# Optimization experiments

Hardware: AMD Instinct MI355X
Metric: run time of the kernel (lower is better)

Reference implementation:

```python
import jax, jax.numpy as jnp
from jax import lax
import numpy as np

B, C, O, K, H, W = 32, 64, 64, 3, 128, 128
COND = 16
DN = ('NCHW', 'OIHW', 'NCHW')


def setup_inputs() -> dict:
    key = jax.random.key(0)
    ks = jax.random.split(key, 12)
    def rn(k, shape, fan_in):
        return jax.random.normal(k, shape, dtype=jnp.float32) / np.sqrt(fan_in)
    return {
        "x": jax.random.normal(ks[0], (B, C, H, W), dtype=jnp.float32),
        # condition_generator: Conv2d(C,16,3,stride=2) -> pool -> relu -> Conv2d(16,16,1) -> relu
        "cg_w1": rn(ks[1], (COND, C, 3, 3), C * 9),
        "cg_b1": jnp.zeros((COND,), jnp.float32),
        "cg_w2": rn(ks[2], (COND, COND), COND),
        "cg_b2": jnp.zeros((COND,), jnp.float32),
        # weight_generator: Conv2d(16, C*K*K, 1) + ReLU
        "wg_w": rn(ks[3], (C * K * K, COND), COND),
        "wg_b": 0.1 * jax.random.normal(ks[4], (C * K * K,), dtype=jnp.float32),
        # pointwise_generator: Conv2d(16, C*O, 1) + ReLU  (channels viewed as [O, C])
        "pg_w": rn(ks[5], (C * O, COND), COND),
        "pg_b": 0.1 * jax.random.normal(ks[6], (C * O,), dtype=jnp.float32),
        # bias_generator: Conv2d(16, O, 1)
        "bg_w": rn(ks[7], (O, COND), COND),
        "bg_b": jnp.zeros((O,), jnp.float32),
        # BatchNorm2d(O) affine params (training-mode batch stats)
        "bn_gamma": jnp.ones((O,), jnp.float32),
        "bn_beta": jnp.zeros((O,), jnp.float32),
    }


def reference(x, cg_w1, cg_b1, cg_w2, cg_b2, wg_w, wg_b, pg_w, pg_b,
              bg_w, bg_b, bn_gamma, bn_beta):
    b, c, h, w = x.shape
    # ---- condition generator: conv3x3 s2 (VALID) -> global avgpool -> relu -> 1x1 -> relu
    cond = lax.conv_general_dilated(x, cg_w1, (2, 2), 'VALID', dimension_numbers=DN)
    cond = cond + cg_b1[None, :, None, None]
    cond = cond.mean(axis=(2, 3))                      # [B,16] (AdaptiveAvgPool2d(1))
    cond = jax.nn.relu(cond)
    cond = jax.nn.relu(cond @ cg_w2.T + cg_b2)         # [B,16]
    # ---- per-sample dynamic weights
    dw = jax.nn.relu(cond @ wg_w.T + wg_b).reshape(b, c, 1, K, K)   # depthwise [B,C,1,K,K]
    pw = jax.nn.relu(cond @ pg_w.T + pg_b).reshape(b, O, c)         # pointwise [B,O,C]
    dbias = cond @ bg_w.T + bg_b                                    # [B,O]
    # ---- per-sample depthwise conv (stride=1, padding=1), vmapped over batch
    def dwconv(xi, ki):  # xi [C,H,W], ki [C,1,K,K]
        return lax.conv_general_dilated(xi[None], ki, (1, 1), [(1, 1), (1, 1)],
                                        feature_group_count=c,
                                        dimension_numbers=DN)[0]
    y = jax.vmap(dwconv)(x, dw)                        # [B,C,H,W]
    # ---- per-sample pointwise 1x1 conv + dynamic bias
    out = jnp.einsum('bchw,boc->bohw', y, pw) + dbias[:, :, None, None]
    # ---- BatchNorm2d (training mode: batch statistics over N,H,W)
    mean = out.mean(axis=(0, 2, 3))
    var = out.var(axis=(0, 2, 3))
    out = (out - mean[None, :, None, None]) * lax.rsqrt(var[None, :, None, None] + 1e-5)
    out = out * bn_gamma[None, :, None, None] + bn_beta[None, :, None, None]
    return out
```

## Files before the change

### kernel.cpp

```cpp
#include <hip/hip_runtime.h>

#define B_ 32
#define C_ 64
#define O_ 64
#define H_ 128
#define W_ 128

typedef __attribute__((ext_vector_type(8))) short short8;
typedef __attribute__((ext_vector_type(4))) float f32x4;

static __device__ __forceinline__ unsigned short f2bf(float f) {
    unsigned u = __builtin_bit_cast(unsigned, f);
    unsigned r = (u + 0x7FFFu + ((u >> 16) & 1u)) >> 16;
    return (unsigned short)r;
}

#define WS_S      0
#define WS_COND2  18432
#define WS_DW     18944
#define WS_DBIAS  37376
#define WS_PWBF   39424
#define WS_PSUM   104960
#define WS_PSQ    236032
#define WS_SCALE  367104
#define WS_SHIFT  367168

__global__ void __launch_bounds__(256) k_strided_sums(const float* __restrict__ x,
                                                      float* __restrict__ Sout) {
    int t = threadIdx.x;
    int bc = blockIdx.x;
    const float4* xp = (const float4*)(x + (size_t)bc * (H_ * W_));
    float a[9];
#pragma unroll
    for (int k = 0; k < 9; k++) a[k] = 0.f;
#pragma unroll
    for (int k = 0; k < 16; k++) {
        int i4 = t + k * 256;
        int h = i4 >> 5;
        int w0 = (i4 & 31) << 2;
        float4 v = xp[i4];
        float mA = (w0 == 124) ? 0.f : 1.f;
        float mB = (w0 == 0) ? 0.f : 1.f;
        float rs0 = v.x + mA * v.z;
        float rs1 = v.y + mA * v.w;
        float rs2 = mB * v.x + v.z;
        float e  = (h & 1) ? 0.f : 1.f;
        float od = 1.f - e;
        float hm0 = (h == 126) ? 0.f : e;
        float hm2 = (h == 0)   ? 0.f : e;
        float hm1 = (h == 127) ? 0.f : od;
        a[0] = fmaf(hm0, rs0, a[0]); a[1] = fmaf(hm0, rs1, a[1]); a[2] = fmaf(hm0, rs2, a[2]);
        a[3] = fmaf(hm1, rs0, a[3]); a[4] = fmaf(hm1, rs1, a[4]); a[5] = fmaf(hm1, rs2, a[5]);
        a[6] = fmaf(hm2, rs0, a[6]); a[7] = fmaf(hm2, rs1, a[7]); a[8] = fmaf(hm2, rs2, a[8]);
    }
    __shared__ float red[4][9];
    int lane = t & 63, wv = t >> 6;
#pragma unroll
    for (int k = 0; k < 9; k++) {
        float v = a[k];
        for (int off = 32; off > 0; off >>= 1) v += __shfl_down(v, off);
        if (lane == 0) red[wv][k] = v;
    }
    __syncthreads();
    if (t < 9) Sout[(size_t)bc * 9 + t] = red[0][t] + red[1][t] + red[2][t] + red[3][t];
}

__global__ void __launch_bounds__(256) k_cond(const float* __restrict__ S,
                       const float* __restrict__ w1, const float* __restrict__ b1,
                       const float* __restrict__ w2, const float* __restrict__ b2,
                       float* __restrict__ cond2) {
    int b = blockIdx.x;
    int t = threadIdx.x;
    int j = t >> 4, seg = t & 15;
    const float* Sb = S + b * 576;
    const float* w1j = w1 + j * 576;
    int i0 = seg * 36;
    float s = 0.f;
#pragma unroll 4
    for (int i = 0; i < 36; i++) s = fmaf(Sb[i0 + i], w1j[i0 + i], s);
    __shared__ float red[16][16];
    __shared__ float condv[16];
    red[j][seg] = s;
    __syncthreads();
    if (t < 16) {
        float acc = 0.f;
#pragma unroll
        for (int k = 0; k < 16; k++) acc += red[t][k];
        acc = acc * (1.f / 3969.f) + b1[t];
        condv[t] = fmaxf(acc, 0.f);
    }
    __syncthreads();
    if (t < 16) {
        float s2 = b2[t];
#pragma unroll
        for (int k = 0; k < 16; k++) s2 = fmaf(condv[k], w2[t * 16 + k], s2);
        cond2[b * 16 + t] = fmaxf(s2, 0.f);
    }
}

__global__ void k_dyn(const float* __restrict__ cond2,
                      const float* __restrict__ wg_w, const float* __restrict__ wg_b,
                      const float* __restrict__ pg_w, const float* __restrict__ pg_b,
                      const float* __restrict__ bg_w, const float* __restrict__ bg_b,
                      float* __restrict__ dw, unsigned short* __restrict__ pwbf,
                      float* __restrict__ dbias) {
    int idx = blockIdx.x * 256 + threadIdx.x;
    if (idx < 18432) {
        int b = idx / 576, r = idx - b * 576;
        const float* cd = cond2 + b * 16;
        float s = wg_b[r];
#pragma unroll
        for (int j = 0; j < 16; j++) s += cd[j] * wg_w[r * 16 + j];
        dw[idx] = fmaxf(s, 0.f);
    } else if (idx < 18432 + 131072) {
        int k = idx - 18432;
        int b = k >> 12, r = k & 4095;
        const float* cd = cond2 + b * 16;
        float s = pg_b[r];
#pragma unroll
        for (int j = 0; j < 16; j++) s += cd[j] * pg_w[r * 16 + j];
        pwbf[k] = f2bf(fmaxf(s, 0.f));
    } else if (idx < 151552) {
        int k = idx - 149504;
        int b = k >> 6, r = k & 63;
        const float* cd = cond2 + b * 16;
        float s = bg_b[r];
#pragma unroll
        for (int j = 0; j < 16; j++) s += cd[j] * bg_w[r * 16 + j];
        dbias[k] = s;
    }
}

struct SM4 {
    union {
        unsigned short y[256 * 72];
        float epi[32 * 260];
    };
    float xr[4 * 4 * 128];
    float dwl[576];
    float sred[256];
    float qred[256];
    float dbl[64];
};

__global__ void __launch_bounds__(256) k_fused(
        const float* __restrict__ x, const float* __restrict__ dw,
        const unsigned short* __restrict__ pwbf, const float* __restrict__ dbias,
        float* __restrict__ out, float* __restrict__ psum, float* __restrict__ psq) {
    __shared__ SM4 sm;
    int t = threadIdx.x;
    int bx = blockIdx.x;
    int b = bx >> 6;
    int pt = bx & 63;
    int h0 = pt << 1;

    int l = t & 63, w_id = t >> 6;
    int quad = l >> 4, l15 = l & 15;

    for (int i = t; i < 576; i += 256) sm.dwl[i] = dw[b * 576 + i];
    if (t < 64) sm.dbl[t] = dbias[b * 64 + t];

    short8 bfr[4][2];
    const unsigned short* pwb = pwbf + (size_t)b * 4096;
#pragma unroll
    for (int nt = 0; nt < 4; nt++)
#pragma unroll
        for (int ck = 0; ck < 2; ck++) {
            int o = nt * 16 + l15;
            int c0 = ck * 32 + quad * 8;
            bfr[nt][ck] = *(const short8*)(pwb + o * 64 + c0);
        }

    f32x4 acc[4][4];
#pragma unroll
    for (int i = 0; i < 4; i++)
#pragma unroll
        for (int j = 0; j < 4; j++) acc[i][j] = (f32x4){0.f, 0.f, 0.f, 0.f};

    int c_loc = t >> 6;
    int pxg = t & 63;
    int px0 = pxg << 2;
    int h_loc = px0 >> 7;
    int w0 = px0 & 127;

    const float* xb = x + ((size_t)b << 20);

    for (int r = 0; r < 16; r++) {
        int cb = r << 2;
        const float* xcb = xb + ((size_t)cb << 14);
#pragma unroll
        for (int k = 0; k < 2; k++) {
            int f4 = t + k * 256;
            int cc = f4 >> 7, rem = f4 & 127;
            int rr = rem >> 5, w4 = rem & 31;
            int hh = h0 - 1 + rr;
            float4 v = make_float4(0.f, 0.f, 0.f, 0.f);
            if (hh >= 0 && hh < 128) v = *(const float4*)(xcb + cc * 16384 + hh * 128 + (w4 << 2));
            *(float4*)&sm.xr[cc * 512 + rr * 128 + (w4 << 2)] = v;
        }
        __syncthreads();

        int cg = cb + c_loc;
        const float* dv = sm.dwl + cg * 9;
        const float* xc = sm.xr + c_loc * 512;
        float y0 = 0.f, y1 = 0.f, y2 = 0.f, y3 = 0.f;
#pragma unroll
        for (int kh = 0; kh < 3; kh++) {
            const float* row = xc + (h_loc + kh) * 128;
            float4 fc = *(const float4*)(row + w0);
            float4 fm = *(const float4*)(row + (w0 ? w0 - 4 : 0));
            float4 fp = *(const float4*)(row + ((w0 < 124) ? w0 + 4 : 120));
            float lft = w0 ? fm.w : 0.f;
            float rgt = (w0 < 124) ? fp.x : 0.f;
            float dA = dv[kh * 3 + 0], dB = dv[kh * 3 + 1], dC = dv[kh * 3 + 2];
            y0 = fmaf(dA, lft, fmaf(dB, fc.x, fmaf(dC, fc.y, y0)));
            y1 = fmaf(dA, fc.x, fmaf(dB, fc.y, fmaf(dC, fc.z, y1)));
            y2 = fmaf(dA, fc.y, fmaf(dB, fc.z, fmaf(dC, fc.w, y2)));
            y3 = fmaf(dA, fc.z, fmaf(dB, fc.w, fmaf(dC, rgt, y3)));
        }
        sm.y[(px0 + 0) * 72 + cg] = f2bf(y0);
        sm.y[(px0 + 1) * 72 + cg] = f2bf(y1);
        sm.y[(px0 + 2) * 72 + cg] = f2bf(y2);
        sm.y[(px0 + 3) * 72 + cg] = f2bf(y3);
        __syncthreads();
    }

    int pxbase = w_id << 6;
#pragma unroll
    for (int ck = 0; ck < 2; ck++) {
        short8 afr[4];
#pragma unroll
        for (int mt = 0; mt < 4; mt++) {
            int px = pxbase + mt * 16 + l15;
            afr[mt] = *(const short8*)&sm.y[px * 72 + ck * 32 + quad * 8];
        }
#pragma unroll
        for (int nt = 0; nt < 4; nt++)
#pragma unroll
            for (int mt = 0; mt < 4; mt++)
                acc[mt][nt] = __builtin_amdgcn_mfma_f32_16x16x32_bf16(
                    afr[mt], bfr[nt][ck], acc[mt][nt], 0, 0, 0);
    }
    __syncthreads();

    float* outb = out + ((size_t)b << 20);
#pragma unroll
    for (int oc = 0; oc < 2; oc++) {
#pragma unroll
        for (int ni = 0; ni < 2; ni++) {
            int nt = oc * 2 + ni;
            int o_loc = ni * 16 + l15;
#pragma unroll
            for (int mt = 0; mt < 4; mt++) {
                int pxw = pxbase + mt * 16 + quad * 4;
                *(f32x4*)&sm.epi[o_loc * 260 + pxw] = acc[mt][nt];
            }
        }
        __syncthreads();
        int o_loc2 = t >> 3;
        int o = oc * 32 + o_loc2;
        int p0 = (t & 7) << 5;
        float dbv = sm.dbl[o];
        float s = 0.f, q = 0.f;
        float* og = outb + (size_t)o * 16384 + h0 * 128 + p0;
#pragma unroll
        for (int i = 0; i < 8; i++) {
            float4 v = *(float4*)&sm.epi[o_loc2 * 260 + p0 + i * 4];
            v.x += dbv; v.y += dbv; v.z += dbv; v.w += dbv;
            s += v.x + v.y + v.z + v.w;
            q += v.x * v.x + v.y * v.y + v.z * v.z + v.w * v.w;
            *(float4*)(og + i * 4) = v;
        }
        sm.sred[t] = s;
        sm.qred[t] = q;
        __syncthreads();
        if (t < 32) {
            float S = 0.f, Q = 0.f;
#pragma unroll
            for (int j2 = 0; j2 < 8; j2++) { S += sm.sred[t * 8 + j2]; Q += sm.qred[t * 8 + j2]; }
            psum[(size_t)bx * 64 + oc * 32 + t] = S;
            psq[(size_t)bx * 64 + oc * 32 + t] = Q;
        }
        __syncthreads();
    }
}

__global__ void k_bnstats(const float* __restrict__ psum, const float* __restrict__ psq,
                          const float* __restrict__ gamma, const float* __restrict__ beta,
                          float* __restrict__ scale, float* __restrict__ shift) {
    int o = blockIdx.x, t = threadIdx.x;
    float s = 0.f, q = 0.f;
    for (int i = t; i < 2048; i += 256) {
        s += psum[(size_t)i * 64 + o];
        q += psq[(size_t)i * 64 + o];
    }
    int lane = t & 63, wv = t >> 6;
    for (int off = 32; off > 0; off >>= 1) { s += __shfl_down(s, off); q += __shfl_down(q, off); }
    __shared__ float rs[4], rq[4];
    if (lane == 0) { rs[wv] = s; rq[wv] = q; }
    __syncthreads();
    if (t == 0) {
        float S = rs[0] + rs[1] + rs[2] + rs[3];
        float Q = rq[0] + rq[1] + rq[2] + rq[3];
        const float invN = 1.f / (float)(B_ * H_ * W_);
        float mean = S * invN;
        float var = fmaxf(Q * invN - mean * mean, 0.f);
        float sc = gamma[o] * rsqrtf(var + 1e-5f);
        scale[o] = sc;
        shift[o] = beta[o] - mean * sc;
    }
}

__global__ void __launch_bounds__(256) k_bnapply(float* __restrict__ out,
                          const float* __restrict__ scale, const float* __restrict__ shift) {
    __shared__ float ss[64], sh[64];
    int t = threadIdx.x;
    if (t < 64) { ss[t] = scale[t]; sh[t] = shift[t]; }
    __syncthreads();
    const int total4 = B_ * O_ * H_ * W_ / 4;
    float4* o4 = (float4*)out;
    for (int i = blockIdx.x * 256 + t; i < total4; i += gridDim.x * 256) {
        int o = (i >> 12) & 63;
        float sc = ss[o], sf = sh[o];
        float4 v = o4[i];
        v.x = fmaf(v.x, sc, sf);
        v.y = fmaf(v.y, sc, sf);
        v.z = fmaf(v.z, sc, sf);
        v.w = fmaf(v.w, sc, sf);
        o4[i] = v;
    }
}

extern "C" void kernel_launch(void* const* d_in, const int* in_sizes, int n_in,
                              void* d_out, int out_size, void* d_ws, size_t ws_size,
                              hipStream_t stream) {
    const float* x     = (const float*)d_in[0];
    const float* cg_w1 = (const float*)d_in[1];
    const float* cg_b1 = (const float*)d_in[2];
    const float* cg_w2 = (const float*)d_in[3];
    const float* cg_b2 = (const float*)d_in[4];
    const float* wg_w  = (const float*)d_in[5];
    const float* wg_b  = (const float*)d_in[6];
    const float* pg_w  = (const float*)d_in[7];
    const float* pg_b  = (const float*)d_in[8];
    const float* bg_w  = (const float*)d_in[9];
    const float* bg_b  = (const float*)d_in[10];
    const float* bn_g  = (const float*)d_in[11];
    const float* bn_b  = (const float*)d_in[12];
    float* out = (float*)d_out;
    float* ws  = (float*)d_ws;

    float* S     = ws + WS_S;
    float* cond2 = ws + WS_COND2;
    float* dw    = ws + WS_DW;
    float* dbias = ws + WS_DBIAS;
    unsigned short* pwbf = (unsigned short*)(ws + WS_PWBF);
    float* psum  = ws + WS_PSUM;
    float* psq   = ws + WS_PSQ;
    float* scale = ws + WS_SCALE;
    float* shift = ws + WS_SHIFT;

    k_strided_sums<<<B_ * C_, 256, 0, stream>>>(x, S);
    k_cond<<<B_, 256, 0, stream>>>(S, cg_w1, cg_b1, cg_w2, cg_b2, cond2);
    k_dyn<<<(151552 + 255) / 256, 256, 0, stream>>>(cond2, wg_w, wg_b, pg_w, pg_b,
                                                    bg_w, bg_b, dw, pwbf, dbias);
    k_fused<<<2048, 256, 0, stream>>>(x, dw, pwbf, dbias, out, psum, psq);
    k_bnstats<<<O_, 256, 0, stream>>>(psum, psq, bn_g, bn_b, scale, shift);
    k_bnapply<<<4096, 256, 0, stream>>>(out, scale, shift);
}
```

Measured before the change: 389.2 us.

## Double-buffer x staging via global_load_lds and restructure fused dwconv/MFMA pipeline

```diff
diff --git a/kernel.cpp b/kernel.cpp
--- a/kernel.cpp
+++ b/kernel.cpp
@@ -7,12 +7,22 @@
 #define W_ 128
 
 typedef __attribute__((ext_vector_type(8))) short short8;
+typedef __attribute__((ext_vector_type(4))) short short4v;
 typedef __attribute__((ext_vector_type(4))) float f32x4;
+
+typedef __attribute__((address_space(1))) const void gv_t;
+typedef __attribute__((address_space(3))) void lv_t;
 
 static __device__ __forceinline__ unsigned short f2bf(float f) {
     unsigned u = __builtin_bit_cast(unsigned, f);
     unsigned r = (u + 0x7FFFu + ((u >> 16) & 1u)) >> 16;
     return (unsigned short)r;
+}
+
+static __device__ __forceinline__ unsigned pk_bf16(float lo, float hi) {
+    unsigned r;
+    asm("v_cvt_pk_bf16_f32 %0, %1, %2" : "=v"(r) : "v"(lo), "v"(hi));
+    return r;
 }
 
 #define WS_S      0
@@ -132,18 +142,15 @@
 }
 
 struct SM4 {
-    union {
-        unsigned short y[256 * 72];
-        float epi[32 * 260];
-    };
-    float xr[4 * 4 * 128];
-    float dwl[576];
-    float sred[256];
-    float qred[256];
+    unsigned short y[256 * 36];
+    float xr[2][4][4][128];
+    float dwl[64 * 12];
+    float sred[4][64];
+    float qred[4][64];
     float dbl[64];
 };
 
-__global__ void __launch_bounds__(256) k_fused(
+__global__ void __launch_bounds__(256, 4) k_fused(
         const float* __restrict__ x, const float* __restrict__ dw,
         const unsigned short* __restrict__ pwbf, const float* __restrict__ dbias,
         float* __restrict__ out, float* __restrict__ psum, float* __restrict__ psq) {
@@ -156,132 +163,163 @@
 
     int l = t & 63, w_id = t >> 6;
     int quad = l >> 4, l15 = l & 15;
-
-    for (int i = t; i < 576; i += 256) sm.dwl[i] = dw[b * 576 + i];
-    if (t < 64) sm.dbl[t] = dbias[b * 64 + t];
-
-    short8 bfr[4][2];
-    const unsigned short* pwb = pwbf + (size_t)b * 4096;
-#pragma unroll
-    for (int nt = 0; nt < 4; nt++)
-#pragma unroll
-        for (int ck = 0; ck < 2; ck++) {
-            int o = nt * 16 + l15;
-            int c0 = ck * 32 + quad * 8;
-            bfr[nt][ck] = *(const short8*)(pwb + o * 64 + c0);
-        }
-
-    f32x4 acc[4][4];
-#pragma unroll
-    for (int i = 0; i < 4; i++)
-#pragma unroll
-        for (int j = 0; j < 4; j++) acc[i][j] = (f32x4){0.f, 0.f, 0.f, 0.f};
-
-    int c_loc = t >> 6;
-    int pxg = t & 63;
-    int px0 = pxg << 2;
+    int pxbase = w_id << 6;
+
+    int m = t & 3;
+    int px0 = t & ~3;
     int h_loc = px0 >> 7;
     int w0 = px0 & 127;
+    float mk0 = (h0 == 0   && h_loc == 0) ? 0.f : 1.f;
+    float mk2 = (h0 == 126 && h_loc == 1) ? 0.f : 1.f;
+
+    for (int i = t; i < 576; i += 256) {
+        int c = i / 9, k = i - c * 9;
+        sm.dwl[c * 12 + k] = dw[b * 576 + i];
+    }
+    if (t < 64) sm.dbl[t] = dbias[b * 64 + t];
 
     const float* xb = x + ((size_t)b << 20);
-
-    for (int r = 0; r < 16; r++) {
-        int cb = r << 2;
-        const float* xcb = xb + ((size_t)cb << 14);
-#pragma unroll
-        for (int k = 0; k < 2; k++) {
-            int f4 = t + k * 256;
+    const unsigned short* pwb = pwbf + (size_t)b * 4096;
+
+    f32x4 acc[4][4];
+#pragma unroll
+    for (int i = 0; i < 4; i++)
+#pragma unroll
+        for (int j = 0; j < 4; j++) acc[i][j] = (f32x4){0.f, 0.f, 0.f, 0.f};
+
+    auto stage = [&](int bf, int cbg) {
+#pragma unroll
+        for (int k2 = 0; k2 < 2; k2++) {
+            int f4 = t + k2 * 256;
             int cc = f4 >> 7, rem = f4 & 127;
             int rr = rem >> 5, w4 = rem & 31;
             int hh = h0 - 1 + rr;
-            float4 v = make_float4(0.f, 0.f, 0.f, 0.f);
-            if (hh >= 0 && hh < 128) v = *(const float4*)(xcb + cc * 16384 + hh * 128 + (w4 << 2));
-            *(float4*)&sm.xr[cc * 512 + rr * 128 + (w4 << 2)] = v;
+            hh = hh < 0 ? 0 : (hh > 127 ? 127 : hh);
+            const float* src = xb + ((size_t)(cbg + cc) << 14) + hh * 128 + (w4 << 2);
+            float* dst = &sm.xr[bf][cc][rr][w4 << 2];
+            __builtin_amdgcn_global_load_lds((gv_t*)src, (lv_t*)dst, 16, 0, 0);
         }
-        __syncthreads();
-
-        int cg = cb + c_loc;
-        const float* dv = sm.dwl + cg * 9;
-        const float* xc = sm.xr + c_loc * 512;
-        float y0 = 0.f, y1 = 0.f, y2 = 0.f, y3 = 0.f;
-#pragma unroll
-        for (int kh = 0; kh < 3; kh++) {
-            const float* row = xc + (h_loc + kh) * 128;
-            float4 fc = *(const float4*)(row + w0);
-            float4 fm = *(const float4*)(row + (w0 ? w0 - 4 : 0));
-            float4 fp = *(const float4*)(row + ((w0 < 124) ? w0 + 4 : 120));
-            float lft = w0 ? fm.w : 0.f;
-            float rgt = (w0 < 124) ? fp.x : 0.f;
-            float dA = dv[kh * 3 + 0], dB = dv[kh * 3 + 1], dC = dv[kh * 3 + 2];
-            y0 = fmaf(dA, lft, fmaf(dB, fc.x, fmaf(dC, fc.y, y0)));
-            y1 = fmaf(dA, fc.x, fmaf(dB, fc.y, fmaf(dC, fc.z, y1)));
-            y2 = fmaf(dA, fc.y, fmaf(dB, fc.z, fmaf(dC, fc.w, y2)));
-            y3 = fmaf(dA, fc.z, fmaf(dB, fc.w, fmaf(dC, rgt, y3)));
+    };
+
+    short8 bfr[4];
+    auto load_bfr = [&](int hf) {
+#pragma unroll
+        for (int nt = 0; nt < 4; nt++) {
+            int o = nt * 16 + l15;
+            bfr[nt] = *(const short8*)(pwb + o * 64 + hf * 32 + quad * 8);
         }
-        sm.y[(px0 + 0) * 72 + cg] = f2bf(y0);
-        sm.y[(px0 + 1) * 72 + cg] = f2bf(y1);
-        sm.y[(px0 + 2) * 72 + cg] = f2bf(y2);
-        sm.y[(px0 + 3) * 72 + cg] = f2bf(y3);
-        __syncthreads();
-    }
-
-    int pxbase = w_id << 6;
-#pragma unroll
-    for (int ck = 0; ck < 2; ck++) {
-        short8 afr[4];
+    };
+
+    auto domfma = [&]() {
+        char* yb = (char*)sm.y;
 #pragma unroll
         for (int mt = 0; mt < 4; mt++) {
             int px = pxbase + mt * 16 + l15;
-            afr[mt] = *(const short8*)&sm.y[px * 72 + ck * 32 + quad * 8];
+            int bofs = px * 72;
+            int sx = px & 7;
+            short4v lo = *(short4v*)(yb + bofs + 8 * ((2 * quad)     ^ sx));
+            short4v hi = *(short4v*)(yb + bofs + 8 * ((2 * quad + 1) ^ sx));
+            short8 a = __builtin_shufflevector(lo, hi, 0, 1, 2, 3, 4, 5, 6, 7);
+#pragma unroll
+            for (int nt = 0; nt < 4; nt++)
+                acc[mt][nt] = __builtin_amdgcn_mfma_f32_16x16x32_bf16(
+                    a, bfr[nt], acc[mt][nt], 0, 0, 0);
         }
-#pragma unroll
-        for (int nt = 0; nt < 4; nt++)
-#pragma unroll
-            for (int mt = 0; mt < 4; mt++)
-                acc[mt][nt] = __builtin_amdgcn_mfma_f32_16x16x32_bf16(
-                    afr[mt], bfr[nt][ck], acc[mt][nt], 0, 0, 0);
-    }
-    __syncthreads();
+    };
+
+    load_bfr(0);
+    stage(0, 0);
+    __syncthreads();
+
+    int buf = 0;
+#pragma unroll
+    for (int idx = 0; idx < 16; idx++) {
+        int cb = idx * 4;
+        int rp = idx & 7;
+        if (idx < 15) stage(buf ^ 1, cb + 4);
+
+        const float* dvp = sm.dwl + (cb + m) * 12;
+        float4 d0 = *(const float4*)(dvp);
+        float4 d1 = *(const float4*)(dvp + 4);
+        float4 d2 = *(const float4*)(dvp + 8);
+        float dA0 = d0.x * mk0, dB0 = d0.y * mk0, dC0 = d0.z * mk0;
+        float dA1 = d0.w,       dB1 = d1.x,       dC1 = d1.y;
+        float dA2 = d1.z * mk2, dB2 = d1.w * mk2, dC2 = d2.x * mk2;
+        const float* xc = &sm.xr[buf][m][0][0];
+        float y0 = 0.f, y1 = 0.f, y2 = 0.f, y3 = 0.f;
+#define STEN(dAx, dBx, dCx, KH) { \
+        const float* row = xc + (h_loc + KH) * 128; \
+        float4 fc = *(const float4*)(row + w0); \
+        float4 fm = *(const float4*)(row + (w0 ? w0 - 4 : 0)); \
+        float4 fp = *(const float4*)(row + ((w0 < 124) ? w0 + 4 : 120)); \
+        float lft = w0 ? fm.w : 0.f; \
+        float rgt = (w0 < 124) ? fp.x : 0.f; \
+        y0 = fmaf(dAx, lft,  fmaf(dBx, fc.x, fmaf(dCx, fc.y, y0))); \
+        y1 = fmaf(dAx, fc.x, fmaf(dBx, fc.y, fmaf(dCx, fc.z, y1))); \
+        y2 = fmaf(dAx, fc.y, fmaf(dBx, fc.z, fmaf(dCx, fc.w, y2))); \
+        y3 = fmaf(dAx, fc.z, fmaf(dBx, fc.w, fmaf(dCx, rgt, y3))); }
+        STEN(dA0, dB0, dC0, 0)
+        STEN(dA1, dB1, dC1, 1)
+        STEN(dA2, dB2, dC2, 2)
+#undef STEN
+
+        unsigned p01 = pk_bf16(y0, y1);
+        unsigned p23 = pk_bf16(y2, y3);
+        bool mhi = (m & 2) != 0;
+        bool mlo = (m & 1) != 0;
+        unsigned send0 = mhi ? p01 : p23;
+        unsigned keep0 = mhi ? p23 : p01;
+        unsigned x2 = (unsigned)__shfl_xor((int)send0, 2);
+        unsigned Lw = mhi ? x2 : keep0;
+        unsigned Hw = mhi ? keep0 : x2;
+        unsigned E0 = (Lw & 0xFFFFu) | (Hw << 16);
+        unsigned E1 = (Lw >> 16) | (Hw & 0xFFFF0000u);
+        unsigned Zk = mlo ? E1 : E0;
+        unsigned Zs = mlo ? E0 : E1;
+        unsigned x1 = (unsigned)__shfl_xor((int)Zs, 1);
+        unsigned Aw = mlo ? x1 : Zk;
+        unsigned Bw = mlo ? Zk : x1;
+        unsigned w01 = (Aw & 0xFFFFu) | (Bw << 16);
+        unsigned w23 = (Aw >> 16) | (Bw & 0xFFFF0000u);
+        int px = px0 | m;
+        int W = px * 72 + 8 * (rp ^ (px & 7));
+        *(uint2*)((char*)sm.y + W) = make_uint2(w01, w23);
+
+        __syncthreads();
+        buf ^= 1;
+        if (idx == 7) {
+            domfma();
+            __syncthreads();
+            load_bfr(1);
+        }
+    }
+    domfma();
 
     float* outb = out + ((size_t)b << 20);
 #pragma unroll
-    for (int oc = 0; oc < 2; oc++) {
-#pragma unroll
-        for (int ni = 0; ni < 2; ni++) {
-            int nt = oc * 2 + ni;
-            int o_loc = ni * 16 + l15;
-#pragma unroll
-            for (int mt = 0; mt < 4; mt++) {
-                int pxw = pxbase + mt * 16 + quad * 4;
-                *(f32x4*)&sm.epi[o_loc * 260 + pxw] = acc[mt][nt];
-            }
-        }
-        __syncthreads();
-        int o_loc2 = t >> 3;
-        int o = oc * 32 + o_loc2;
-        int p0 = (t & 7) << 5;
+    for (int nt = 0; nt < 4; nt++) {
+        int o = nt * 16 + l15;
         float dbv = sm.dbl[o];
         float s = 0.f, q = 0.f;
-        float* og = outb + (size_t)o * 16384 + h0 * 128 + p0;
-#pragma unroll
-        for (int i = 0; i < 8; i++) {
-            float4 v = *(float4*)&sm.epi[o_loc2 * 260 + p0 + i * 4];
-            v.x += dbv; v.y += dbv; v.z += dbv; v.w += dbv;
+        float* og = outb + (size_t)o * 16384 + h0 * 128 + pxbase + quad * 4;
+#pragma unroll
+        for (int mt = 0; mt < 4; mt++) {
+            f32x4 a = acc[mt][nt];
+            float4 v = make_float4(a.x + dbv, a.y + dbv, a.z + dbv, a.w + dbv);
             s += v.x + v.y + v.z + v.w;
             q += v.x * v.x + v.y * v.y + v.z * v.z + v.w * v.w;
-            *(float4*)(og + i * 4) = v;
+            *(float4*)(og + mt * 16) = v;
         }
-        sm.sred[t] = s;
-        sm.qred[t] = q;
-        __syncthreads();
-        if (t < 32) {
-            float S = 0.f, Q = 0.f;
-#pragma unroll
-            for (int j2 = 0; j2 < 8; j2++) { S += sm.sred[t * 8 + j2]; Q += sm.qred[t * 8 + j2]; }
-            psum[(size_t)bx * 64 + oc * 32 + t] = S;
-            psq[(size_t)bx * 64 + oc * 32 + t] = Q;
-        }
-        __syncthreads();
+        s += __shfl_xor(s, 16); s += __shfl_xor(s, 32);
+        q += __shfl_xor(q, 16); q += __shfl_xor(q, 32);
+        if (l < 16) { sm.sred[w_id][o] = s; sm.qred[w_id][o] = q; }
+    }
+    __syncthreads();
+    if (t < 64) {
+        float S = sm.sred[0][t] + sm.sred[1][t] + sm.sred[2][t] + sm.sred[3][t];
+        float Q = sm.qred[0][t] + sm.qred[1][t] + sm.qred[2][t] + sm.qred[3][t];
+        psum[(size_t)bx * 64 + t] = S;
+        psq[(size_t)bx * 64 + t] = Q;
     }
 }
 
```

After: 361.9 us. -7.0%, faster.
